# Optimization experiments

Hardware: AMD Instinct MI355X
Metric: run time of the kernel (lower is better)

The kernel has to match this reference:

```python
import jax, jax.numpy as jnp
import numpy as np

NEG_SLOPE = 0.01  # nn.LeakyReLU default

N = 100000
E = 1600000
D_IN = 128
D_OUT = 128


def setup_inputs() -> dict:
    key = jax.random.key(0)
    ks = jax.random.split(key, 8)
    features = jax.random.normal(ks[0], (N, D_IN), dtype=jnp.float32)
    adj_rows = jax.random.randint(ks[1], (E,), 0, N, dtype=jnp.int64)
    adj_cols = jax.random.randint(ks[2], (E,), 0, N, dtype=jnp.int64)
    adj_vals = jax.random.uniform(ks[3], (E,), dtype=jnp.float32)
    s1 = 1.0 / np.sqrt(D_IN)
    W1 = jax.random.uniform(ks[4], (D_IN, D_OUT), jnp.float32, -s1, s1)
    b1 = jax.random.uniform(ks[5], (D_OUT,), jnp.float32, -s1, s1)
    W2 = jax.random.uniform(ks[6], (D_IN, D_OUT), jnp.float32, -s1, s1)
    b2 = jax.random.uniform(ks[7], (D_OUT,), jnp.float32, -s1, s1)
    return {"features": features, "adj_rows": adj_rows, "adj_cols": adj_cols,
            "adj_vals": adj_vals, "W1": W1, "b1": b1, "W2": W2, "b2": b2}


def reference(features, adj_rows, adj_cols, adj_vals, W1, b1, W2, b2):
    # h_neigh = adj @ features  (COO SpMM via gather + segment_sum)
    msgs = adj_vals[:, None] * features[adj_cols]          # [E, D_IN]
    h_neigh = jax.ops.segment_sum(msgs, adj_rows, num_segments=features.shape[0])
    term1 = (features + h_neigh) @ W1 + b1                 # W1(features + h_neigh)
    term2 = (features * h_neigh) @ W2 + b2                 # W2(features * h_neigh)
    pre = term1 + term2
    return jnp.where(pre >= 0, pre, NEG_SLOPE * pre)       # leaky_relu
```

## Files before the change

kernel.cpp:

```cpp
#include <hip/hip_runtime.h>

#define D 128
#define BM 64
#define CAP 3072

typedef short short8 __attribute__((ext_vector_type(8)));
typedef unsigned short ushort8_t __attribute__((ext_vector_type(8)));
typedef float f32x4 __attribute__((ext_vector_type(4)));

__device__ __forceinline__ unsigned short f2bf(float x) {
    unsigned u = __float_as_uint(x);
    unsigned r = (u + 0x7fffu + ((u >> 16) & 1u)) >> 16;
    return (unsigned short)r;
}
__device__ __forceinline__ float bf2f(unsigned short u) {
    return __uint_as_float(((unsigned)u) << 16);
}

__global__ __launch_bounds__(256) void prep_kernel(
    const float4* __restrict__ feat4, ushort4* __restrict__ fbf4, int nf4,
    const float* __restrict__ W1, const float* __restrict__ W2,
    unsigned short* __restrict__ WT,
    const int* __restrict__ rows, int* __restrict__ bcnt,
    int E, int nb, int epb)
{
    __shared__ int cnt[1024];
    const int t = threadIdx.x;
    const int b = blockIdx.x;
    for (int i = t; i < nb; i += 256) cnt[i] = 0;
    __syncthreads();

    int e0 = b * epb;
    int e1 = e0 + epb; if (e1 > E) e1 = E;
    for (int e = e0 + t; e < e1; e += 256) atomicAdd(&cnt[rows[e] >> 7], 1);

    for (int i = b * 256 + t; i < nf4; i += 256 * 256) {
        float4 v = feat4[i];
        fbf4[i] = make_ushort4(f2bf(v.x), f2bf(v.y), f2bf(v.z), f2bf(v.w));
    }

    if (b < 128) {
        int idx = b * 256 + t;
        int c = idx & 127;
        int k = idx >> 7;
        float w = (k < 128) ? W1[k * 128 + c] : W2[(k - 128) * 128 + c];
        WT[c * 256 + k] = f2bf(w);
    }

    __syncthreads();
    for (int i = t; i < nb; i += 256)
        if (cnt[i]) atomicAdd(&bcnt[i], cnt[i]);
}

__global__ __launch_bounds__(256) void fconv_kernel(
    const float4* __restrict__ feat4, ushort4* __restrict__ fbf4, int total)
{
    int i = blockIdx.x * 256 + threadIdx.x;
    if (i < total) {
        float4 v = feat4[i];
        fbf4[i] = make_ushort4(f2bf(v.x), f2bf(v.y), f2bf(v.z), f2bf(v.w));
    }
}

__global__ __launch_bounds__(256) void wconv_kernel(
    const float* __restrict__ W1, const float* __restrict__ W2,
    unsigned short* __restrict__ WT)
{
    int idx = blockIdx.x * 256 + threadIdx.x;
    int c = idx & 127;
    int k = idx >> 7;
    float w = (k < 128) ? W1[k * 128 + c] : W2[(k - 128) * 128 + c];
    WT[c * 256 + k] = f2bf(w);
}

__global__ __launch_bounds__(1024) void bucket_scan_kernel(
    const int* __restrict__ bcnt, int* __restrict__ bstart,
    int* __restrict__ bcur, int nb, int E)
{
    __shared__ int wsum[16];
    int tid = threadIdx.x, lane = tid & 63, wid = tid >> 6;
    int x = (tid < nb) ? bcnt[tid] : 0;
    int v = x;
    #pragma unroll
    for (int off = 1; off < 64; off <<= 1) {
        int y = __shfl_up(v, off, 64);
        if (lane >= off) v += y;
    }
    if (lane == 63) wsum[wid] = v;
    __syncthreads();
    if (wid == 0 && lane < 16) {
        int s = wsum[lane];
        #pragma unroll
        for (int off = 1; off < 16; off <<= 1) {
            int y = __shfl_up(s, off, 64);
            if (lane >= off) s += y;
        }
        wsum[lane] = s;
    }
    __syncthreads();
    int wexcl = wid ? wsum[wid - 1] : 0;
    int excl = wexcl + v - x;
    if (tid < nb) { bstart[tid] = excl; bcur[tid] = excl; }
    if (tid == 0) bstart[nb] = E;
}

__global__ __launch_bounds__(256) void bucket_scatter_kernel(
    const int* __restrict__ rows, const int* __restrict__ cols,
    const float* __restrict__ vals, int* __restrict__ bcur,
    uint2* __restrict__ bsedge, int E, int nb)
{
    __shared__ int cnt[1024];
    __shared__ int base[1024];
    int t = threadIdx.x;
    int e0 = blockIdx.x * 4096;
    for (int i = t; i < nb; i += 256) cnt[i] = 0;
    __syncthreads();
    #pragma unroll
    for (int q = 0; q < 16; ++q) {
        int e = e0 + t + q * 256;
        if (e < E) atomicAdd(&cnt[rows[e] >> 7], 1);
    }
    __syncthreads();
    for (int i = t; i < nb; i += 256) {
        int c = cnt[i];
        if (c) { base[i] = atomicAdd(&bcur[i], c); cnt[i] = 0; }
    }
    __syncthreads();
    #pragma unroll
    for (int q = 0; q < 16; ++q) {
        int e = e0 + t + q * 256;
        if (e < E) {
            int r = rows[e];
            int b = r >> 7;
            int pos = base[b] + atomicAdd(&cnt[b], 1);
            bsedge[pos] = make_uint2(((unsigned)(r & 127) << 17) | (unsigned)cols[e],
                                     __float_as_uint(vals[e]));
        }
    }
}

__global__ __launch_bounds__(512) void spmm_sort_ab_kernel(
    const ushort8_t* __restrict__ fbf8,
    const int* __restrict__ bstart,
    const uint2* __restrict__ bsedge,
    unsigned char* __restrict__ ambf, int N)
{
    __shared__ uint2 sL[CAP];
    __shared__ int cnt[128];
    __shared__ int base[129];

    const int t = threadIdx.x;
    const int b = blockIdx.x;
    const int s = bstart[b], e = bstart[b + 1];
    const int M = e - s;

    if (t < 128) cnt[t] = 0;
    __syncthreads();
    for (int j = s + t; j < e; j += 512)
        atomicAdd(&cnt[bsedge[j].x >> 17], 1);
    __syncthreads();
    if (t < 64) {
        int c0 = cnt[2 * t], c1 = cnt[2 * t + 1];
        int pair = c0 + c1;
        int v = pair;
        #pragma unroll
        for (int off = 1; off < 64; off <<= 1) {
            int y = __shfl_up(v, off, 64);
            if (t >= off) v += y;
        }
        int excl = v - pair;
        base[2 * t]     = excl;
        base[2 * t + 1] = excl + c0;
        if (t == 63) base[128] = excl + pair;
        cnt[2 * t] = 0;
        cnt[2 * t + 1] = 0;
    }
    __syncthreads();

    const int g = t >> 4;
    const int l = t & 15;

    if (M <= CAP) {
        for (int j = s + t; j < e; j += 512) {
            uint2 ed = bsedge[j];
            int rl = ed.x >> 17;
            int p = atomicAdd(&cnt[rl], 1);
            sL[base[rl] + p] = make_uint2(ed.x & 0x1FFFFu, ed.y);
        }
        __syncthreads();

        #pragma unroll
        for (int rr = 0; rr < 4; ++rr) {
            int rl = g + rr * 32;
            int row = (b << 7) + rl;
            if (row >= N) continue;
            int j  = base[rl];
            int j1 = base[rl + 1];
            float acc[8] = {};
            for (; j + 3 < j1; j += 4) {
                uint2 e0 = sL[j],     e1 = sL[j + 1];
                uint2 e2 = sL[j + 2], e3 = sL[j + 3];
                ushort8_t f0 = fbf8[(size_t)e0.x * 16 + l];
                ushort8_t f1 = fbf8[(size_t)e1.x * 16 + l];
                ushort8_t f2 = fbf8[(size_t)e2.x * 16 + l];
                ushort8_t f3 = fbf8[(size_t)e3.x * 16 + l];
                float v0 = __uint_as_float(e0.y), v1 = __uint_as_float(e1.y);
                float v2 = __uint_as_float(e2.y), v3 = __uint_as_float(e3.y);
                #pragma unroll
                for (int q = 0; q < 8; ++q) {
                    acc[q] = fmaf(v0, bf2f(f0[q]), acc[q]);
                    acc[q] = fmaf(v1, bf2f(f1[q]), acc[q]);
                    acc[q] = fmaf(v2, bf2f(f2[q]), acc[q]);
                    acc[q] = fmaf(v3, bf2f(f3[q]), acc[q]);
                }
            }
            for (; j < j1; ++j) {
                uint2 e0 = sL[j];
                float v = __uint_as_float(e0.y);
                ushort8_t f0 = fbf8[(size_t)e0.x * 16 + l];
                #pragma unroll
                for (int q = 0; q < 8; ++q) acc[q] = fmaf(v, bf2f(f0[q]), acc[q]);
            }

            ushort8_t fown = fbf8[(size_t)row * 16 + l];
            ushort8_t av, mv;
            #pragma unroll
            for (int q = 0; q < 8; ++q) {
                float f = bf2f(fown[q]);
                av[q] = f2bf(f + acc[q]);
                mv[q] = f2bf(f * acc[q]);
            }
            int swz = (row & 7) << 4;
            unsigned char* rowp = ambf + (size_t)row * 512;
            *(ushort8_t*)(rowp + ((16 * l) ^ swz))       = av;
            *(ushort8_t*)(rowp + 256 + ((16 * l) ^ swz)) = mv;
        }
    } else {
        #pragma unroll
        for (int rr = 0; rr < 4; ++rr) {
            int rl = g + rr * 32;
            int row = (b << 7) + rl;
            if (row >= N) continue;
            float acc[8] = {};
            for (int j = s; j < e; ++j) {
                uint2 ed = bsedge[j];
                if ((int)(ed.x >> 17) == rl) {
                    float v = __uint_as_float(ed.y);
                    ushort8_t f0 = fbf8[(size_t)(ed.x & 0x1FFFFu) * 16 + l];
                    #pragma unroll
                    for (int q = 0; q < 8; ++q) acc[q] = fmaf(v, bf2f(f0[q]), acc[q]);
                }
            }
            ushort8_t fown = fbf8[(size_t)row * 16 + l];
            ushort8_t av, mv;
            #pragma unroll
            for (int q = 0; q < 8; ++q) {
                float f = bf2f(fown[q]);
                av[q] = f2bf(f + acc[q]);
                mv[q] = f2bf(f * acc[q]);
            }
            int swz = (row & 7) << 4;
            unsigned char* rowp = ambf + (size_t)row * 512;
            *(ushort8_t*)(rowp + ((16 * l) ^ swz))       = av;
            *(ushort8_t*)(rowp + 256 + ((16 * l) ^ swz)) = mv;
        }
    }
}

__global__ __launch_bounds__(256) void mfma_gemm2_kernel(
    const unsigned char* __restrict__ ambf,
    const unsigned short* __restrict__ WT,
    const float* __restrict__ b1, const float* __restrict__ b2,
    float* __restrict__ out, int N)
{
    __shared__ __align__(16) unsigned char am_raw[64 * 512];

    const int tid = threadIdx.x;
    const int block0 = blockIdx.x * BM;

    const short8* src = (const short8*)(ambf + (size_t)block0 * 512);
    short8* dst = (short8*)am_raw;
    #pragma unroll
    for (int it = 0; it < 8; ++it) {
        int idx = tid + it * 256;
        dst[idx] = src[idx];
    }
    __syncthreads();

    const int lane = tid & 63;
    const int w    = tid >> 6;
    const int wr   = w >> 1;
    const int wc   = w & 1;
    const int l15  = lane & 15;
    const int lk   = lane >> 4;
    const int rswz = (l15 & 7) << 4;

    f32x4 acc[2][4] = {};

    const char* WTc = (const char*)WT;
    const unsigned char* arow0 = am_raw + (wr * 32 + l15) * 512;
    const unsigned char* arow1 = arow0 + 16 * 512;

    #pragma unroll
    for (int ks = 0; ks < 8; ++ks) {
        int kbyte = ks * 64 + lk * 16;
        int akoff = kbyte ^ rswz;
        short8 a0 = *(const short8*)(arow0 + akoff);
        short8 a1 = *(const short8*)(arow1 + akoff);
        short8 bfr[4];
        #pragma unroll
        for (int nc = 0; nc < 4; ++nc) {
            int col = wc * 64 + nc * 16 + l15;
            bfr[nc] = *(const short8*)(WTc + col * 512 + kbyte);
        }
        #pragma unroll
        for (int nc = 0; nc < 4; ++nc) {
            acc[0][nc] = __builtin_amdgcn_mfma_f32_16x16x32_bf16(a0, bfr[nc], acc[0][nc], 0, 0, 0);
            acc[1][nc] = __builtin_amdgcn_mfma_f32_16x16x32_bf16(a1, bfr[nc], acc[1][nc], 0, 0, 0);
        }
    }

    #pragma unroll
    for (int nc = 0; nc < 4; ++nc) {
        int col = wc * 64 + nc * 16 + l15;
        float bias = b1[col] + b2[col];
        #pragma unroll
        for (int mr = 0; mr < 2; ++mr) {
            int rbase = block0 + wr * 32 + mr * 16 + lk * 4;
            #pragma unroll
            for (int r = 0; r < 4; ++r) {
                int row = rbase + r;
                if (row < N) {
                    float v = acc[mr][nc][r] + bias;
                    out[row * 128 + col] = (v >= 0.f) ? v : 0.01f * v;
                }
            }
        }
    }
}

__global__ __launch_bounds__(256) void bucket_sort_kernel(
    const uint2* __restrict__ bsedge,
    const int* __restrict__ bstart,
    uint2* __restrict__ sedge,
    int* __restrict__ row_start,
    int N, int E)
{
    __shared__ int cnt[128];
    __shared__ int base[128];
    const int b = blockIdx.x;
    const int t = threadIdx.x;
    const int s = bstart[b], e = bstart[b + 1];
    if (t < 128) cnt[t] = 0;
    __syncthreads();
    for (int j = s + t; j < e; j += 256)
        atomicAdd(&cnt[bsedge[j].x >> 17], 1);
    __syncthreads();
    if (t < 64) {
        int c0 = cnt[2 * t], c1 = cnt[2 * t + 1];
        int pair = c0 + c1;
        int v = pair;
        #pragma unroll
        for (int off = 1; off < 64; off <<= 1) {
            int y = __shfl_up(v, off, 64);
            if (t >= off) v += y;
        }
        int excl = v - pair;
        base[2 * t]     = excl;
        base[2 * t + 1] = excl + c0;
        cnt[2 * t] = 0;
        cnt[2 * t + 1] = 0;
    }
    __syncthreads();
    const int r0 = b << 7;
    if (t < 128 && r0 + t < N) row_start[r0 + t] = s + base[t];
    if (b == 0 && t == 0) row_start[N] = E;
    for (int j = s + t; j < e; j += 256) {
        uint2 ed = bsedge[j];
        int rl = ed.x >> 17;
        int p = atomicAdd(&cnt[rl], 1);
        sedge[s + base[rl] + p] = make_uint2(ed.x & 0x1FFFFu, ed.y);
    }
}

__global__ __launch_bounds__(256) void spmm_ab_kernel(
    const ushort8_t* __restrict__ fbf8,
    const int* __restrict__ row_start,
    const uint2* __restrict__ sedge,
    unsigned char* __restrict__ ambf, int N)
{
    int t = blockIdx.x * 256 + threadIdx.x;
    int row  = t >> 5;
    int half = (t >> 4) & 1;
    int l    = t & 15;
    if (row >= N) return;

    int s = row_start[row];
    int e = row_start[row + 1];
    int mid = s + ((e - s + 1) >> 1);
    int j0 = half ? mid : s;
    int j1 = half ? e : mid;

    float acc[8] = {};
    int j = j0;
    for (; j + 3 < j1; j += 4) {
        uint2 e0 = sedge[j],     e1 = sedge[j + 1];
        uint2 e2 = sedge[j + 2], e3 = sedge[j + 3];
        ushort8_t f0 = fbf8[(size_t)e0.x * 16 + l];
        ushort8_t f1 = fbf8[(size_t)e1.x * 16 + l];
        ushort8_t f2 = fbf8[(size_t)e2.x * 16 + l];
        ushort8_t f3 = fbf8[(size_t)e3.x * 16 + l];
        float v0 = __uint_as_float(e0.y), v1 = __uint_as_float(e1.y);
        float v2 = __uint_as_float(e2.y), v3 = __uint_as_float(e3.y);
        #pragma unroll
        for (int q = 0; q < 8; ++q) {
            acc[q] = fmaf(v0, bf2f(f0[q]), acc[q]);
            acc[q] = fmaf(v1, bf2f(f1[q]), acc[q]);
            acc[q] = fmaf(v2, bf2f(f2[q]), acc[q]);
            acc[q] = fmaf(v3, bf2f(f3[q]), acc[q]);
        }
    }
    for (; j < j1; ++j) {
        uint2 e0 = sedge[j];
        float v = __uint_as_float(e0.y);
        ushort8_t f0 = fbf8[(size_t)e0.x * 16 + l];
        #pragma unroll
        for (int q = 0; q < 8; ++q) acc[q] = fmaf(v, bf2f(f0[q]), acc[q]);
    }

    #pragma unroll
    for (int q = 0; q < 8; ++q)
        acc[q] += __shfl_xor(acc[q], 16, 64);

    if (half == 0) {
        ushort8_t fown = fbf8[(size_t)row * 16 + l];
        ushort8_t av, mv;
        #pragma unroll
        for (int q = 0; q < 8; ++q) {
            float f = bf2f(fown[q]);
            av[q] = f2bf(f + acc[q]);
            mv[q] = f2bf(f * acc[q]);
        }
        int swz = (row & 7) << 4;
        unsigned char* rowp = ambf + (size_t)row * 512;
        *(ushort8_t*)(rowp + ((16 * l) ^ swz))       = av;
        *(ushort8_t*)(rowp + 256 + ((16 * l) ^ swz)) = mv;
    }
}

__global__ __launch_bounds__(256) void hist_kernel(
    const int* __restrict__ rows, int* __restrict__ counts, int E)
{
    int e = blockIdx.x * 256 + threadIdx.x;
    if (e < E) atomicAdd(&counts[rows[e]], 1);
}

__global__ __launch_bounds__(256) void scan_pass1(
    const int* __restrict__ counts, int* __restrict__ btot, int N)
{
    int tid = threadIdx.x;
    int i = blockIdx.x * 1024 + tid * 4;
    int s = 0;
    if (i + 3 < N) {
        int4 v = *(const int4*)(counts + i);
        s = v.x + v.y + v.z + v.w;
    } else {
        for (int q = 0; q < 4; ++q) if (i + q < N) s += counts[i + q];
    }
    #pragma unroll
    for (int off = 32; off >= 1; off >>= 1) s += __shfl_down(s, off, 64);
    __shared__ int ws[4];
    if ((tid & 63) == 0) ws[tid >> 6] = s;
    __syncthreads();
    if (tid == 0) btot[blockIdx.x] = ws[0] + ws[1] + ws[2] + ws[3];
}

__global__ __launch_bounds__(1024) void scan_pass2(
    const int* __restrict__ btot, int* __restrict__ boff, int nb)
{
    __shared__ int wsum[16];
    int tid = threadIdx.x, lane = tid & 63, wid = tid >> 6;
    int x = (tid < nb) ? btot[tid] : 0;
    int v = x;
    #pragma unroll
    for (int off = 1; off < 64; off <<= 1) {
        int y = __shfl_up(v, off, 64);
        if (lane >= off) v += y;
    }
    if (lane == 63) wsum[wid] = v;
    __syncthreads();
    if (wid == 0 && lane < 16) {
        int s = wsum[lane];
        #pragma unroll
        for (int off = 1; off < 16; off <<= 1) {
            int y = __shfl_up(s, off, 64);
            if (lane >= off) s += y;
        }
        wsum[lane] = s;
    }
    __syncthreads();
    int wexcl = wid ? wsum[wid - 1] : 0;
    if (tid < nb) boff[tid] = wexcl + v - x;
}

__global__ __launch_bounds__(256) void scan_pass3(
    int* __restrict__ row_start, int* __restrict__ cursor,
    const int* __restrict__ boff, int N, int E)
{
    int tid = threadIdx.x;
    int base = blockIdx.x * 1024 + tid * 4;
    int c0 = 0, c1 = 0, c2 = 0, c3 = 0;
    if (base + 3 < N) {
        int4 v = *(const int4*)(row_start + base);
        c0 = v.x; c1 = v.y; c2 = v.z; c3 = v.w;
    } else {
        if (base + 0 < N) c0 = row_start[base + 0];
        if (base + 1 < N) c1 = row_start[base + 1];
        if (base + 2 < N) c2 = row_start[base + 2];
        if (base + 3 < N) c3 = row_start[base + 3];
    }
    int s0 = c0, s1 = s0 + c1, s2 = s1 + c2, s3 = s2 + c3;
    int lane = tid & 63, wid = tid >> 6;
    int v = s3;
    #pragma unroll
    for (int off = 1; off < 64; off <<= 1) {
        int y = __shfl_up(v, off, 64);
        if (lane >= off) v += y;
    }
    __shared__ int ws[4];
    if (lane == 63) ws[wid] = v;
    __syncthreads();
    int wexcl = 0;
    for (int q = 0; q < wid; ++q) wexcl += ws[q];
    int texcl = wexcl + (v - s3) + boff[blockIdx.x];
    int e0 = texcl, e1 = texcl + s0, e2 = texcl + s1, e3 = texcl + s2;
    if (base + 0 < N) { row_start[base + 0] = e0; cursor[base + 0] = e0; }
    if (base + 1 < N) { row_start[base + 1] = e1; cursor[base + 1] = e1; }
    if (base + 2 < N) { row_start[base + 2] = e2; cursor[base + 2] = e2; }
    if (base + 3 < N) { row_start[base + 3] = e3; cursor[base + 3] = e3; }
    if (blockIdx.x == 0 && tid == 0) row_start[N] = E;
}

__global__ __launch_bounds__(256) void scatter_sort_kernel(
    const int* __restrict__ rows, const int* __restrict__ cols,
    const float* __restrict__ vals, int* __restrict__ cursor,
    uint2* __restrict__ sedge, int E)
{
    int e = blockIdx.x * 256 + threadIdx.x;
    if (e < E) {
        int r = rows[e];
        int p = atomicAdd(&cursor[r], 1);
        sedge[p] = make_uint2((unsigned)cols[e], __float_as_uint(vals[e]));
    }
}

__global__ __launch_bounds__(256) void spmm_kernel(
    const float2* __restrict__ feat2,
    const int* __restrict__ row_start,
    const uint2* __restrict__ sedge,
    float2* __restrict__ h2, int N)
{
    int gw = (blockIdx.x * 256 + threadIdx.x) >> 6;
    int lane = threadIdx.x & 63;
    if (gw >= N) return;
    int s = row_start[gw];
    int e = row_start[gw + 1];
    float2 acc = make_float2(0.f, 0.f);
    int j = s;
    for (; j + 1 < e; j += 2) {
        uint2 e0 = sedge[j], e1 = sedge[j + 1];
        float v0 = __uint_as_float(e0.y), v1 = __uint_as_float(e1.y);
        float2 f0 = feat2[(size_t)e0.x * 64 + lane];
        float2 f1 = feat2[(size_t)e1.x * 64 + lane];
        acc.x = fmaf(v0, f0.x, acc.x);
        acc.y = fmaf(v0, f0.y, acc.y);
        acc.x = fmaf(v1, f1.x, acc.x);
        acc.y = fmaf(v1, f1.y, acc.y);
    }
    if (j < e) {
        uint2 e0 = sedge[j];
        float v = __uint_as_float(e0.y);
        float2 f = feat2[(size_t)e0.x * 64 + lane];
        acc.x = fmaf(v, f.x, acc.x);
        acc.y = fmaf(v, f.y, acc.y);
    }
    h2[(size_t)gw * 64 + lane] = acc;
}

__global__ __launch_bounds__(256) void mfma_gemm_kernel(
    const float4* __restrict__ feat4, const float4* __restrict__ h4,
    const unsigned short* __restrict__ WT,
    const float* __restrict__ b1, const float* __restrict__ b2,
    float* __restrict__ out, int N)
{
    __shared__ __align__(16) unsigned char am_raw[64 * 512];
    const int tid = threadIdx.x;
    const int block0 = blockIdx.x * BM;
    #pragma unroll
    for (int it = 0; it < 8; ++it) {
        int idx  = tid + it * 256;
        int node = idx >> 5;
        int p    = idx & 31;
        int g    = block0 + node;
        float4 fv = make_float4(0.f, 0.f, 0.f, 0.f);
        float4 hv = make_float4(0.f, 0.f, 0.f, 0.f);
        if (g < N) { fv = feat4[g * 32 + p]; hv = h4[g * 32 + p]; }
        ushort4 av = make_ushort4(f2bf(fv.x + hv.x), f2bf(fv.y + hv.y),
                                  f2bf(fv.z + hv.z), f2bf(fv.w + hv.w));
        ushort4 mv = make_ushort4(f2bf(fv.x * hv.x), f2bf(fv.y * hv.y),
                                  f2bf(fv.z * hv.z), f2bf(fv.w * hv.w));
        int swz = (node & 7) << 4;
        *(ushort4*)(am_raw + node * 512 + ((p * 8) ^ swz))       = av;
        *(ushort4*)(am_raw + node * 512 + ((256 + p * 8) ^ swz)) = mv;
    }
    __syncthreads();
    const int lane = tid & 63;
    const int w    = tid >> 6;
    const int wr   = w >> 1;
    const int wc   = w & 1;
    const int l15  = lane & 15;
    const int lk   = lane >> 4;
    const int rswz = (l15 & 7) << 4;
    f32x4 acc[2][4] = {};
    const char* WTc = (const char*)WT;
    const unsigned char* arow0 = am_raw + (wr * 32 + l15) * 512;
    const unsigned char* arow1 = arow0 + 16 * 512;
    #pragma unroll
    for (int ks = 0; ks < 8; ++ks) {
        int kbyte = ks * 64 + lk * 16;
        int akoff = kbyte ^ rswz;
        short8 a0 = *(const short8*)(arow0 + akoff);
        short8 a1 = *(const short8*)(arow1 + akoff);
        short8 bfr[4];
        #pragma unroll
        for (int nc = 0; nc < 4; ++nc) {
            int col = wc * 64 + nc * 16 + l15;
            bfr[nc] = *(const short8*)(WTc + col * 512 + kbyte);
        }
        #pragma unroll
        for (int nc = 0; nc < 4; ++nc) {
            acc[0][nc] = __builtin_amdgcn_mfma_f32_16x16x32_bf16(a0, bfr[nc], acc[0][nc], 0, 0, 0);
            acc[1][nc] = __builtin_amdgcn_mfma_f32_16x16x32_bf16(a1, bfr[nc], acc[1][nc], 0, 0, 0);
        }
    }
    #pragma unroll
    for (int nc = 0; nc < 4; ++nc) {
        int col = wc * 64 + nc * 16 + l15;
        float bias = b1[col] + b2[col];
        #pragma unroll
        for (int mr = 0; mr < 2; ++mr) {
            int rbase = block0 + wr * 32 + mr * 16 + lk * 4;
            #pragma unroll
            for (int r = 0; r < 4; ++r) {
                int row = rbase + r;
                if (row < N) {
                    float v = acc[mr][nc][r] + bias;
                    out[row * 128 + col] = (v >= 0.f) ? v : 0.01f * v;
                }
            }
        }
    }
}

__global__ __launch_bounds__(256) void edge_scatter_kernel(
    const float4* __restrict__ feat4, const int* __restrict__ rows,
    const int* __restrict__ cols, const float* __restrict__ vals,
    float* __restrict__ h, int E)
{
    int idx = blockIdx.x * 256 + threadIdx.x;
    if (idx >= E * 32) return;
    int e = idx >> 5;
    int p = idx & 31;
    int r = rows[e];
    int c = cols[e];
    float v = vals[e];
    float4 f = feat4[c * 32 + p];
    float* hr = h + (long long)r * D + p * 4;
    unsafeAtomicAdd(hr + 0, v * f.x);
    unsafeAtomicAdd(hr + 1, v * f.y);
    unsafeAtomicAdd(hr + 2, v * f.z);
    unsafeAtomicAdd(hr + 3, v * f.w);
}

__global__ __launch_bounds__(256) void fused_gemm_kernel(
    const float* __restrict__ feat, const float* __restrict__ h,
    const float* __restrict__ W1, const float* __restrict__ b1,
    const float* __restrict__ W2, const float* __restrict__ b2,
    float* __restrict__ out, int N)
{
    __shared__ float a_lds[BM][D];
    __shared__ float m_lds[BM][D];
    const int tid = threadIdx.x;
    const int block0 = blockIdx.x * BM;
    const float4* feat4 = (const float4*)feat;
    const float4* h4    = (const float4*)h;
    #pragma unroll
    for (int it = 0; it < 8; ++it) {
        int idx  = tid + it * 256;
        int node = idx >> 5;
        int p    = idx & 31;
        int gnode = block0 + node;
        float4 fv = make_float4(0.f, 0.f, 0.f, 0.f);
        float4 hv = make_float4(0.f, 0.f, 0.f, 0.f);
        if (gnode < N) { fv = feat4[gnode * 32 + p]; hv = h4[gnode * 32 + p]; }
        float4 av = make_float4(fv.x + hv.x, fv.y + hv.y, fv.z + hv.z, fv.w + hv.w);
        float4 mv = make_float4(fv.x * hv.x, fv.y * hv.y, fv.z * hv.z, fv.w * hv.w);
        *(float4*)&a_lds[node][p * 4] = av;
        *(float4*)&m_lds[node][p * 4] = mv;
    }
    __syncthreads();
    const int c = tid & 31;
    const int g = tid >> 5;
    float acc[8][4] = {};
    const float4* W1v = (const float4*)W1;
    const float4* W2v = (const float4*)W2;
    for (int k = 0; k < D; ++k) {
        float4 w1 = W1v[k * 32 + c];
        float4 w2 = W2v[k * 32 + c];
        #pragma unroll
        for (int t = 0; t < 8; ++t) {
            float av = a_lds[g + 8 * t][k];
            float mv = m_lds[g + 8 * t][k];
            acc[t][0] = fmaf(av, w1.x, fmaf(mv, w2.x, acc[t][0]));
            acc[t][1] = fmaf(av, w1.y, fmaf(mv, w2.y, acc[t][1]));
            acc[t][2] = fmaf(av, w1.z, fmaf(mv, w2.z, acc[t][2]));
            acc[t][3] = fmaf(av, w1.w, fmaf(mv, w2.w, acc[t][3]));
        }
    }
    float4 bb1 = ((const float4*)b1)[c];
    float4 bb2 = ((const float4*)b2)[c];
    const float bx = bb1.x + bb2.x, by = bb1.y + bb2.y;
    const float bz = bb1.z + bb2.z, bw = bb1.w + bb2.w;
    #pragma unroll
    for (int t = 0; t < 8; ++t) {
        int gnode = block0 + g + 8 * t;
        if (gnode >= N) continue;
        float4 o;
        o.x = acc[t][0] + bx; o.y = acc[t][1] + by;
        o.z = acc[t][2] + bz; o.w = acc[t][3] + bw;
        o.x = (o.x >= 0.f) ? o.x : 0.01f * o.x;
        o.y = (o.y >= 0.f) ? o.y : 0.01f * o.y;
        o.z = (o.z >= 0.f) ? o.z : 0.01f * o.z;
        o.w = (o.w >= 0.f) ? o.w : 0.01f * o.w;
        ((float4*)out)[gnode * 32 + c] = o;
    }
}

extern "C" void kernel_launch(void* const* d_in, const int* in_sizes, int n_in,
                              void* d_out, int out_size, void* d_ws, size_t ws_size,
                              hipStream_t stream) {
    const float* feat = (const float*)d_in[0];
    const int*   rows = (const int*)d_in[1];
    const int*   cols = (const int*)d_in[2];
    const float* vals = (const float*)d_in[3];
    const float* W1   = (const float*)d_in[4];
    const float* b1   = (const float*)d_in[5];
    const float* W2   = (const float*)d_in[6];
    const float* b2   = (const float*)d_in[7];

    const int N = in_sizes[0] / D;
    const int E = in_sizes[1];
    float* out = (float*)d_out;

    const int NBK  = (N + 127) >> 7;
    const int Npad = NBK << 7;

    size_t off = 0;
    unsigned char* ambf = (unsigned char*)d_ws;                    off += (size_t)Npad * 512;
    unsigned short* featbf = (unsigned short*)((char*)d_ws + off); off += (size_t)N * D * 2;
    off = (off + 15) & ~(size_t)15;
    unsigned short* WT = (unsigned short*)((char*)d_ws + off);     off += 128 * 256 * 2;
    off = (off + 15) & ~(size_t)15;
    uint2* bsedge = (uint2*)((char*)d_ws + off);                   off += (size_t)E * 8;
    int* bcnt   = (int*)((char*)d_ws + off);                       off += (size_t)NBK * 4;
    int* bstart = (int*)((char*)d_ws + off);                       off += (size_t)(NBK + 1) * 4;
    int* bcur   = (int*)((char*)d_ws + off);                       off += (size_t)NBK * 4;
    size_t need1a = off;

    if (ws_size >= need1a && NBK <= 1024 && N <= (1 << 17)) {
        hipMemsetAsync(bcnt, 0, (size_t)NBK * sizeof(int), stream);
        int epb = (E + 255) / 256;
        prep_kernel<<<256, 256, 0, stream>>>(
            (const float4*)feat, (ushort4*)featbf, N * 32,
            W1, W2, WT, rows, bcnt, E, NBK, epb);
        bucket_scan_kernel<<<1, 1024, 0, stream>>>(bcnt, bstart, bcur, NBK, E);
        bucket_scatter_kernel<<<(E + 4095) / 4096, 256, 0, stream>>>(
            rows, cols, vals, bcur, bsedge, E, NBK);
        spmm_sort_ab_kernel<<<NBK, 512, 0, stream>>>(
            (const ushort8_t*)featbf, bstart, bsedge, ambf, N);
        mfma_gemm2_kernel<<<(N + BM - 1) / BM, 256, 0, stream>>>(
            ambf, WT, b1, b2, out, N);
        return;
    }

    off = 0;
    ambf = (unsigned char*)d_ws;                                   off += (size_t)Npad * 512;
    featbf = (unsigned short*)((char*)d_ws + off);                 off += (size_t)N * D * 2;
    off = (off + 15) & ~(size_t)15;
    uint2* sedge = (uint2*)((char*)d_ws + off);                    off += (size_t)E * 8;
    WT = (unsigned short*)((char*)d_ws + off);                     off += 128 * 256 * 2;
    int* row_start = (int*)((char*)d_ws + off);                    off += (size_t)(N + 1) * 4;
    off = (off + 15) & ~(size_t)15;
    bsedge = (uint2*)((char*)d_ws + off);                          off += (size_t)E * 8;
    bcnt   = (int*)((char*)d_ws + off);                            off += (size_t)NBK * 4;
    bstart = (int*)((char*)d_ws + off);                            off += (size_t)(NBK + 1) * 4;
    bcur   = (int*)((char*)d_ws + off);                            off += (size_t)NBK * 4;
    size_t need1b = off;

    if (ws_size >= need1b && NBK <= 1024 && N <= (1 << 17)) {
        hipMemsetAsync(bcnt, 0, (size_t)NBK * sizeof(int), stream);
        int epb = (E + 255) / 256;
        prep_kernel<<<256, 256, 0, stream>>>(
            (const float4*)feat, (ushort4*)featbf, N * 32,
            W1, W2, WT, rows, bcnt, E, NBK, epb);
        bucket_scan_kernel<<<1, 1024, 0, stream>>>(bcnt, bstart, bcur, NBK, E);
        bucket_scatter_kernel<<<(E + 4095) / 4096, 256, 0, stream>>>(
            rows, cols, vals, bcur, bsedge, E, NBK);
        bucket_sort_kernel<<<NBK, 256, 0, stream>>>(
            bsedge, bstart, sedge, row_start, N, E);
        spmm_ab_kernel<<<((size_t)N * 32 + 255) / 256, 256, 0, stream>>>(
            (const ushort8_t*)featbf, row_start, sedge, ambf, N);
        mfma_gemm2_kernel<<<(N + BM - 1) / BM, 256, 0, stream>>>(
            ambf, WT, b1, b2, out, N);
        return;
    }

    const int NB = (N + 1023) / 1024;
    off = 0;
    float* h = (float*)d_ws;                           off += (size_t)N * D * 4;
    int* row_start2 = (int*)((char*)d_ws + off);       off += (size_t)(N + 1) * 4;
    int* cursor2    = (int*)((char*)d_ws + off);       off += (size_t)N * 4;
    off = (off + 15) & ~(size_t)15;
    uint2* sedge2   = (uint2*)((char*)d_ws + off);     off += (size_t)E * 8;
    off = (off + 15) & ~(size_t)15;
    unsigned short* WT2 = (unsigned short*)((char*)d_ws + off); off += 128 * 256 * 2;
    int* btot2 = (int*)((char*)d_ws + off);            off += (size_t)NB * 4;
    int* boff2 = (int*)((char*)d_ws + off);            off += (size_t)NB * 4;
    size_t need2 = off;

    if (ws_size >= need2 && NB <= 1024) {
        hipMemsetAsync(row_start2, 0, (size_t)(N + 1) * sizeof(int), stream);
        wconv_kernel<<<128, 256, 0, stream>>>(W1, W2, WT2);
        hist_kernel<<<(E + 255) / 256, 256, 0, stream>>>(rows, row_start2, E);
        scan_pass1<<<NB, 256, 0, stream>>>(row_start2, btot2, N);
        scan_pass2<<<1, 1024, 0, stream>>>(btot2, boff2, NB);
        scan_pass3<<<NB, 256, 0, stream>>>(row_start2, cursor2, boff2, N, E);
        scatter_sort_kernel<<<(E + 255) / 256, 256, 0, stream>>>(
            rows, cols, vals, cursor2, sedge2, E);
        spmm_kernel<<<(N * 64 + 255) / 256, 256, 0, stream>>>(
            (const float2*)feat, row_start2, sedge2, (float2*)h, N);
        mfma_gemm_kernel<<<(N + BM - 1) / BM, 256, 0, stream>>>(
            (const float4*)feat, (const float4*)h, WT2, b1, b2, out, N);
        return;
    }

    size_t hbytes = (size_t)N * D * sizeof(float);
    float* hh = (ws_size >= hbytes) ? (float*)d_ws : out;
    hipMemsetAsync(hh, 0, hbytes, stream);
    edge_scatter_kernel<<<((size_t)E * 32 + 255) / 256, 256, 0, stream>>>(
        (const float4*)feat, rows, cols, vals, hh, E);
    fused_gemm_kernel<<<(N + BM - 1) / BM, 256, 0, stream>>>(
        feat, hh, W1, b1, W2, b2, out, N);
}
```

Before: 185.0 us.

## Split each 128-row bucket across two 64-row SpMM blocks

Replaces the per-bucket SpMM kernel with a version that launches two blocks per 128-row bucket, each handling one 64-row half with a smaller shared-memory edge list. Each block scans the whole bucket but keeps only its half's edges, so edge reads double while per-block LDS shrinks and the grid doubles, aiming at higher occupancy and better load balance. The fallback path (bucket_sort + per-row spmm) is removed, and a slow linear-scan path handles halves that overflow the LDS capacity.

```diff
diff --git a/kernel.cpp b/kernel.cpp
--- a/kernel.cpp
+++ b/kernel.cpp
@@ -3,6 +3,7 @@
 #define D 128
 #define BM 64
 #define CAP 3072
+#define CAP2 1792
 
 typedef short short8 __attribute__((ext_vector_type(8)));
 typedef unsigned short ushort8_t __attribute__((ext_vector_type(8)));
@@ -135,6 +136,211 @@
             int pos = base[b] + atomicAdd(&cnt[b], 1);
             bsedge[pos] = make_uint2(((unsigned)(r & 127) << 17) | (unsigned)cols[e],
                                      __float_as_uint(vals[e]));
+        }
+    }
+}
+
+__global__ __launch_bounds__(512) void spmm_sort_ab64_kernel(
+    const ushort8_t* __restrict__ fbf8,
+    const int* __restrict__ bstart,
+    const uint2* __restrict__ bsedge,
+    unsigned char* __restrict__ ambf, int N)
+{
+    __shared__ uint2 sL[CAP2];
+    __shared__ int cnt[64];
+    __shared__ int base[65];
+
+    const int t  = threadIdx.x;
+    const int bb = blockIdx.x;
+    const int bk = bb >> 1;
+    const int hs = bb & 1;
+    const int s = bstart[bk], e = bstart[bk + 1];
+
+    if (t < 64) cnt[t] = 0;
+    __syncthreads();
+    for (int j = s + t; j < e; j += 512) {
+        int rl = bsedge[j].x >> 17;
+        if ((rl >> 6) == hs) atomicAdd(&cnt[rl & 63], 1);
+    }
+    __syncthreads();
+    if (t < 64) {
+        int c = cnt[t];
+        int v = c;
+        #pragma unroll
+        for (int off = 1; off < 64; off <<= 1) {
+            int y = __shfl_up(v, off, 64);
+            if (t >= off) v += y;
+        }
+        base[t] = v - c;
+        if (t == 63) base[64] = v;
+        cnt[t] = 0;
+    }
+    __syncthreads();
+    const int Mh = base[64];
+
+    const int g = t >> 4;
+    const int l = t & 15;
+    const int row0 = (bk << 7) + (hs << 6);
+
+    if (Mh <= CAP2) {
+        for (int j = s + t; j < e; j += 512) {
+            uint2 ed = bsedge[j];
+            int rl = ed.x >> 17;
+            if ((rl >> 6) == hs) {
+                int r6 = rl & 63;
+                int p = atomicAdd(&cnt[r6], 1);
+                sL[base[r6] + p] = make_uint2(ed.x & 0x1FFFFu, ed.y);
+            }
+        }
+        __syncthreads();
+
+        #pragma unroll
+        for (int rr = 0; rr < 2; ++rr) {
+            int r6 = g + rr * 32;
+            int row = row0 + r6;
+            if (row >= N) continue;
+            int j  = base[r6];
+            int j1 = base[r6 + 1];
+            float acc[8] = {};
+            for (; j + 3 < j1; j += 4) {
+                uint2 e0 = sL[j],     e1 = sL[j + 1];
+                uint2 e2 = sL[j + 2], e3 = sL[j + 3];
+                ushort8_t f0 = fbf8[(size_t)e0.x * 16 + l];
+                ushort8_t f1 = fbf8[(size_t)e1.x * 16 + l];
+                ushort8_t f2 = fbf8[(size_t)e2.x * 16 + l];
+                ushort8_t f3 = fbf8[(size_t)e3.x * 16 + l];
+                float v0 = __uint_as_float(e0.y), v1 = __uint_as_float(e1.y);
+                float v2 = __uint_as_float(e2.y), v3 = __uint_as_float(e3.y);
+                #pragma unroll
+                for (int q = 0; q < 8; ++q) {
+                    acc[q] = fmaf(v0, bf2f(f0[q]), acc[q]);
+                    acc[q] = fmaf(v1, bf2f(f1[q]), acc[q]);
+                    acc[q] = fmaf(v2, bf2f(f2[q]), acc[q]);
+                    acc[q] = fmaf(v3, bf2f(f3[q]), acc[q]);
+                }
+            }
+            for (; j < j1; ++j) {
+                uint2 e0 = sL[j];
+                float v = __uint_as_float(e0.y);
+                ushort8_t f0 = fbf8[(size_t)e0.x * 16 + l];
+                #pragma unroll
+                for (int q = 0; q < 8; ++q) acc[q] = fmaf(v, bf2f(f0[q]), acc[q]);
+            }
+
+            ushort8_t fown = fbf8[(size_t)row * 16 + l];
+            ushort8_t av, mv;
+            #pragma unroll
+            for (int q = 0; q < 8; ++q) {
+                float f = bf2f(fown[q]);
+                av[q] = f2bf(f + acc[q]);
+                mv[q] = f2bf(f * acc[q]);
+            }
+            int swz = (row & 7) << 4;
+            unsigned char* rowp = ambf + (size_t)row * 512;
+            *(ushort8_t*)(rowp + ((16 * l) ^ swz))       = av;
+            *(ushort8_t*)(rowp + 256 + ((16 * l) ^ swz)) = mv;
+        }
+    } else {
+        #pragma unroll
+        for (int rr = 0; rr < 2; ++rr) {
+            int r6 = g + rr * 32;
+            int row = row0 + r6;
+            if (row >= N) continue;
+            int rlwant = (hs << 6) + r6;
+            float acc[8] = {};
+            for (int j = s; j < e; ++j) {
+                uint2 ed = bsedge[j];
+                if ((int)(ed.x >> 17) == rlwant) {
+                    float v = __uint_as_float(ed.y);
+                    ushort8_t f0 = fbf8[(size_t)(ed.x & 0x1FFFFu) * 16 + l];
+                    #pragma unroll
+                    for (int q = 0; q < 8; ++q) acc[q] = fmaf(v, bf2f(f0[q]), acc[q]);
+                }
+            }
+            ushort8_t fown = fbf8[(size_t)row * 16 + l];
+            ushort8_t av, mv;
+            #pragma unroll
+            for (int q = 0; q < 8; ++q) {
+                float f = bf2f(fown[q]);
+                av[q] = f2bf(f + acc[q]);
+                mv[q] = f2bf(f * acc[q]);
+            }
+            int swz = (row & 7) << 4;
+            unsigned char* rowp = ambf + (size_t)row * 512;
+            *(ushort8_t*)(rowp + ((16 * l) ^ swz))       = av;
+            *(ushort8_t*)(rowp + 256 + ((16 * l) ^ swz)) = mv;
+        }
+    }
+}
+
+__global__ __launch_bounds__(256) void mfma_gemm2_kernel(
+    const unsigned char* __restrict__ ambf,
+    const unsigned short* __restrict__ WT,
+    const float* __restrict__ b1, const float* __restrict__ b2,
+    float* __restrict__ out, int N)
+{
+    __shared__ __align__(16) unsigned char am_raw[64 * 512];
+
+    const int tid = threadIdx.x;
+    const int block0 = blockIdx.x * BM;
+
+    const short8* src = (const short8*)(ambf + (size_t)block0 * 512);
+    short8* dst = (short8*)am_raw;
+    #pragma unroll
+    for (int it = 0; it < 8; ++it) {
+        int idx = tid + it * 256;
+        dst[idx] = src[idx];
+    }
+    __syncthreads();
+
+    const int lane = tid & 63;
+    const int w    = tid >> 6;
+    const int wr   = w >> 1;
+    const int wc   = w & 1;
+    const int l15  = lane & 15;
+    const int lk   = lane >> 4;
+    const int rswz = (l15 & 7) << 4;
+
+    f32x4 acc[2][4] = {};
+
+    const char* WTc = (const char*)WT;
+    const unsigned char* arow0 = am_raw + (wr * 32 + l15) * 512;
+    const unsigned char* arow1 = arow0 + 16 * 512;
+
+    #pragma unroll
+    for (int ks = 0; ks < 8; ++ks) {
+        int kbyte = ks * 64 + lk * 16;
+        int akoff = kbyte ^ rswz;
+        short8 a0 = *(const short8*)(arow0 + akoff);
+        short8 a1 = *(const short8*)(arow1 + akoff);
+        short8 bfr[4];
+        #pragma unroll
+        for (int nc = 0; nc < 4; ++nc) {
+            int col = wc * 64 + nc * 16 + l15;
+            bfr[nc] = *(const short8*)(WTc + col * 512 + kbyte);
+        }
+        #pragma unroll
+        for (int nc = 0; nc < 4; ++nc) {
+            acc[0][nc] = __builtin_amdgcn_mfma_f32_16x16x32_bf16(a0, bfr[nc], acc[0][nc], 0, 0, 0);
+            acc[1][nc] = __builtin_amdgcn_mfma_f32_16x16x32_bf16(a1, bfr[nc], acc[1][nc], 0, 0, 0);
+        }
+    }
+
+    #pragma unroll
+    for (int nc = 0; nc < 4; ++nc) {
+        int col = wc * 64 + nc * 16 + l15;
+        float bias = b1[col] + b2[col];
+        #pragma unroll
+        for (int mr = 0; mr < 2; ++mr) {
+            int rbase = block0 + wr * 32 + mr * 16 + lk * 4;
+            #pragma unroll
+            for (int r = 0; r < 4; ++r) {
+                int row = rbase + r;
+                if (row < N) {
+                    float v = acc[mr][nc][r] + bias;
+                    out[row * 128 + col] = (v >= 0.f) ? v : 0.01f * v;
+                }
+            }
         }
     }
 }
@@ -267,187 +473,6 @@
     }
 }
 
-__global__ __launch_bounds__(256) void mfma_gemm2_kernel(
-    const unsigned char* __restrict__ ambf,
-    const unsigned short* __restrict__ WT,
-    const float* __restrict__ b1, const float* __restrict__ b2,
-    float* __restrict__ out, int N)
-{
-    __shared__ __align__(16) unsigned char am_raw[64 * 512];
-
-    const int tid = threadIdx.x;
-    const int block0 = blockIdx.x * BM;
-
-    const short8* src = (const short8*)(ambf + (size_t)block0 * 512);
-    short8* dst = (short8*)am_raw;
-    #pragma unroll
-    for (int it = 0; it < 8; ++it) {
-        int idx = tid + it * 256;
-        dst[idx] = src[idx];
-    }
-    __syncthreads();
-
-    const int lane = tid & 63;
-    const int w    = tid >> 6;
-    const int wr   = w >> 1;
-    const int wc   = w & 1;
-    const int l15  = lane & 15;
-    const int lk   = lane >> 4;
-    const int rswz = (l15 & 7) << 4;
-
-    f32x4 acc[2][4] = {};
-
-    const char* WTc = (const char*)WT;
-    const unsigned char* arow0 = am_raw + (wr * 32 + l15) * 512;
-    const unsigned char* arow1 = arow0 + 16 * 512;
-
-    #pragma unroll
-    for (int ks = 0; ks < 8; ++ks) {
-        int kbyte = ks * 64 + lk * 16;
-        int akoff = kbyte ^ rswz;
-        short8 a0 = *(const short8*)(arow0 + akoff);
-        short8 a1 = *(const short8*)(arow1 + akoff);
-        short8 bfr[4];
-        #pragma unroll
-        for (int nc = 0; nc < 4; ++nc) {
-            int col = wc * 64 + nc * 16 + l15;
-            bfr[nc] = *(const short8*)(WTc + col * 512 + kbyte);
-        }
-        #pragma unroll
-        for (int nc = 0; nc < 4; ++nc) {
-            acc[0][nc] = __builtin_amdgcn_mfma_f32_16x16x32_bf16(a0, bfr[nc], acc[0][nc], 0, 0, 0);
-            acc[1][nc] = __builtin_amdgcn_mfma_f32_16x16x32_bf16(a1, bfr[nc], acc[1][nc], 0, 0, 0);
-        }
-    }
-
-    #pragma unroll
-    for (int nc = 0; nc < 4; ++nc) {
-        int col = wc * 64 + nc * 16 + l15;
-        float bias = b1[col] + b2[col];
-        #pragma unroll
-        for (int mr = 0; mr < 2; ++mr) {
-            int rbase = block0 + wr * 32 + mr * 16 + lk * 4;
-            #pragma unroll
-            for (int r = 0; r < 4; ++r) {
-                int row = rbase + r;
-                if (row < N) {
-                    float v = acc[mr][nc][r] + bias;
-                    out[row * 128 + col] = (v >= 0.f) ? v : 0.01f * v;
-                }
-            }
-        }
-    }
-}
-
-__global__ __launch_bounds__(256) void bucket_sort_kernel(
-    const uint2* __restrict__ bsedge,
-    const int* __restrict__ bstart,
-    uint2* __restrict__ sedge,
-    int* __restrict__ row_start,
-    int N, int E)
-{
-    __shared__ int cnt[128];
-    __shared__ int base[128];
-    const int b = blockIdx.x;
-    const int t = threadIdx.x;
-    const int s = bstart[b], e = bstart[b + 1];
-    if (t < 128) cnt[t] = 0;
-    __syncthreads();
-    for (int j = s + t; j < e; j += 256)
-        atomicAdd(&cnt[bsedge[j].x >> 17], 1);
-    __syncthreads();
-    if (t < 64) {
-        int c0 = cnt[2 * t], c1 = cnt[2 * t + 1];
-        int pair = c0 + c1;
-        int v = pair;
-        #pragma unroll
-        for (int off = 1; off < 64; off <<= 1) {
-            int y = __shfl_up(v, off, 64);
-            if (t >= off) v += y;
-        }
-        int excl = v - pair;
-        base[2 * t]     = excl;
-        base[2 * t + 1] = excl + c0;
-        cnt[2 * t] = 0;
-        cnt[2 * t + 1] = 0;
-    }
-    __syncthreads();
-    const int r0 = b << 7;
-    if (t < 128 && r0 + t < N) row_start[r0 + t] = s + base[t];
-    if (b == 0 && t == 0) row_start[N] = E;
-    for (int j = s + t; j < e; j += 256) {
-        uint2 ed = bsedge[j];
-        int rl = ed.x >> 17;
-        int p = atomicAdd(&cnt[rl], 1);
-        sedge[s + base[rl] + p] = make_uint2(ed.x & 0x1FFFFu, ed.y);
-    }
-}
-
-__global__ __launch_bounds__(256) void spmm_ab_kernel(
-    const ushort8_t* __restrict__ fbf8,
-    const int* __restrict__ row_start,
-    const uint2* __restrict__ sedge,
-    unsigned char* __restrict__ ambf, int N)
-{
-    int t = blockIdx.x * 256 + threadIdx.x;
-    int row  = t >> 5;
-    int half = (t >> 4) & 1;
-    int l    = t & 15;
-    if (row >= N) return;
-
-    int s = row_start[row];
-    int e = row_start[row + 1];
-    int mid = s + ((e - s + 1) >> 1);
-    int j0 = half ? mid : s;
-    int j1 = half ? e : mid;
-
-    float acc[8] = {};
-    int j = j0;
-    for (; j + 3 < j1; j += 4) {
-        uint2 e0 = sedge[j],     e1 = sedge[j + 1];
-        uint2 e2 = sedge[j + 2], e3 = sedge[j + 3];
-        ushort8_t f0 = fbf8[(size_t)e0.x * 16 + l];
-        ushort8_t f1 = fbf8[(size_t)e1.x * 16 + l];
-        ushort8_t f2 = fbf8[(size_t)e2.x * 16 + l];
-        ushort8_t f3 = fbf8[(size_t)e3.x * 16 + l];
-        float v0 = __uint_as_float(e0.y), v1 = __uint_as_float(e1.y);
-        float v2 = __uint_as_float(e2.y), v3 = __uint_as_float(e3.y);
-        #pragma unroll
-        for (int q = 0; q < 8; ++q) {
-            acc[q] = fmaf(v0, bf2f(f0[q]), acc[q]);
-            acc[q] = fmaf(v1, bf2f(f1[q]), acc[q]);
-            acc[q] = fmaf(v2, bf2f(f2[q]), acc[q]);
-            acc[q] = fmaf(v3, bf2f(f3[q]), acc[q]);
-        }
-    }
-    for (; j < j1; ++j) {
-        uint2 e0 = sedge[j];
-        float v = __uint_as_float(e0.y);
-        ushort8_t f0 = fbf8[(size_t)e0.x * 16 + l];
-        #pragma unroll
-        for (int q = 0; q < 8; ++q) acc[q] = fmaf(v, bf2f(f0[q]), acc[q]);
-    }
-
-    #pragma unroll
-    for (int q = 0; q < 8; ++q)
-        acc[q] += __shfl_xor(acc[q], 16, 64);
-
-    if (half == 0) {
-        ushort8_t fown = fbf8[(size_t)row * 16 + l];
-        ushort8_t av, mv;
-        #pragma unroll
-        for (int q = 0; q < 8; ++q) {
-            float f = bf2f(fown[q]);
-            av[q] = f2bf(f + acc[q]);
-            mv[q] = f2bf(f * acc[q]);
-        }
-        int swz = (row & 7) << 4;
-        unsigned char* rowp = ambf + (size_t)row * 512;
-        *(ushort8_t*)(rowp + ((16 * l) ^ swz))       = av;
-        *(ushort8_t*)(rowp + 256 + ((16 * l) ^ swz)) = mv;
-    }
-}
-
 __global__ __launch_bounds__(256) void hist_kernel(
     const int* __restrict__ rows, int* __restrict__ counts, int E)
 {
@@ -775,9 +800,9 @@
     int* bcnt   = (int*)((char*)d_ws + off);                       off += (size_t)NBK * 4;
     int* bstart = (int*)((char*)d_ws + off);                       off += (size_t)(NBK + 1) * 4;
     int* bcur   = (int*)((char*)d_ws + off);                       off += (size_t)NBK * 4;
-    size_t need1a = off;
-
-    if (ws_size >= need1a && NBK <= 1024 && N <= (1 << 17)) {
+    size_t need1 = off;
+
+    if (ws_size >= need1 && NBK <= 1024 && N <= (1 << 17)) {
         hipMemsetAsync(bcnt, 0, (size_t)NBK * sizeof(int), stream);
         int epb = (E + 255) / 256;
         prep_kernel<<<256, 256, 0, stream>>>(
@@ -786,40 +811,8 @@
         bucket_scan_kernel<<<1, 1024, 0, stream>>>(bcnt, bstart, bcur, NBK, E);
         bucket_scatter_kernel<<<(E + 4095) / 4096, 256, 0, stream>>>(
             rows, cols, vals, bcur, bsedge, E, NBK);
-        spmm_sort_ab_kernel<<<NBK, 512, 0, stream>>>(
+        spmm_sort_ab64_kernel<<<NBK * 2, 512, 0, stream>>>(
             (const ushort8_t*)featbf, bstart, bsedge, ambf, N);
-        mfma_gemm2_kernel<<<(N + BM - 1) / BM, 256, 0, stream>>>(
-            ambf, WT, b1, b2, out, N);
-        return;
-    }
-
-    off = 0;
-    ambf = (unsigned char*)d_ws;                                   off += (size_t)Npad * 512;
-    featbf = (unsigned short*)((char*)d_ws + off);                 off += (size_t)N * D * 2;
-    off = (off + 15) & ~(size_t)15;
-    uint2* sedge = (uint2*)((char*)d_ws + off);                    off += (size_t)E * 8;
-    WT = (unsigned short*)((char*)d_ws + off);                     off += 128 * 256 * 2;
-    int* row_start = (int*)((char*)d_ws + off);                    off += (size_t)(N + 1) * 4;
-    off = (off + 15) & ~(size_t)15;
-    bsedge = (uint2*)((char*)d_ws + off);                          off += (size_t)E * 8;
-    bcnt   = (int*)((char*)d_ws + off);                            off += (size_t)NBK * 4;
-    bstart = (int*)((char*)d_ws + off);                            off += (size_t)(NBK + 1) * 4;
-    bcur   = (int*)((char*)d_ws + off);                            off += (size_t)NBK * 4;
-    size_t need1b = off;
-
-    if (ws_size >= need1b && NBK <= 1024 && N <= (1 << 17)) {
-        hipMemsetAsync(bcnt, 0, (size_t)NBK * sizeof(int), stream);
-        int epb = (E + 255) / 256;
-        prep_kernel<<<256, 256, 0, stream>>>(
-            (const float4*)feat, (ushort4*)featbf, N * 32,
-            W1, W2, WT, rows, bcnt, E, NBK, epb);
-        bucket_scan_kernel<<<1, 1024, 0, stream>>>(bcnt, bstart, bcur, NBK, E);
-        bucket_scatter_kernel<<<(E + 4095) / 4096, 256, 0, stream>>>(
-            rows, cols, vals, bcur, bsedge, E, NBK);
-        bucket_sort_kernel<<<NBK, 256, 0, stream>>>(
-            bsedge, bstart, sedge, row_start, N, E);
-        spmm_ab_kernel<<<((size_t)N * 32 + 255) / 256, 256, 0, stream>>>(
-            (const ushort8_t*)featbf, row_start, sedge, ambf, N);
         mfma_gemm2_kernel<<<(N + BM - 1) / BM, 256, 0, stream>>>(
             ambf, WT, b1, b2, out, N);
         return;
```

New measurement: 182.0 us. About the same (-1.6%).
